# Performance work log

Measured on AMD Instinct MI355X. Metric: run time of the kernel, lower is better.

The kernel has to match this reference:

```python
import jax, jax.numpy as jnp
import numpy as np

IN_D = 512
VOCAB = 32000
SEQ = 2048

def setup_inputs() -> dict:
    key = jax.random.key(0)
    ks = jax.random.split(key, 12)
    d = IN_D
    def xavier(k, shape):
        fan_in, fan_out = shape[1], shape[0]
        a = jnp.sqrt(6.0 / (fan_in + fan_out))
        return jax.random.uniform(k, shape, jnp.float32, -a, a)
    return {
        'X': jax.random.randint(ks[0], (1, SEQ), 0, VOCAB),
        'wz': xavier(ks[1], (VOCAB, d)),
        'uz': xavier(ks[2], (d, d)),
        'w': xavier(ks[3], (VOCAB, d)),
        'u': xavier(ks[4], (d, d)),
        'wr': xavier(ks[5], (VOCAB, d)),
        'ur': xavier(ks[6], (d, d)),
        'wy': xavier(ks[7], (VOCAB, d)),
        'bz': xavier(ks[8], (1, d)),
        'br': xavier(ks[9], (1, d)),
        'bh': xavier(ks[10], (1, d)),
        'by': xavier(ks[11], (1, VOCAB)),
    }

def reference(X, wz, uz, w, u, wr, ur, wy, bz, br, bh, by):
    idx = X[0]                      # (T,) batch is hardcoded to 1 in original
    ez = wz[idx]                    # (T, d) per-step embedding gathers, done once
    er = wr[idx]
    eh = w[idx]

    def step(h, emb):
        e_z, e_r, e_h = emb
        z = jax.nn.sigmoid(e_z + h @ uz.T + bz[0])
        r = jax.nn.sigmoid(e_r + h @ ur.T + br[0])
        h_xh = jnp.tanh(e_h + (r * h) @ u.T + bh[0])
        h_new = h * z + (1.0 - z) * h_xh
        return h_new, h_new

    h0 = jnp.zeros((wz.shape[1],), dtype=wz.dtype)
    _, hs = jax.lax.scan(step, h0, (ez, er, eh))   # hs: (T, d)
    logits = hs @ wy.T + by[0]                     # (T, vocab)
    outs = jax.nn.log_softmax(logits, axis=-1)     # matches squeeze(0)
    hiddens = hs[None, :, :]                       # (1, T, d)
    return outs, hiddens
```

## Files before the change

### kernel.cpp

```cpp
#include <hip/hip_runtime.h>
#include <math.h>

typedef unsigned short u16;
typedef unsigned long long u64;
typedef unsigned short us8 __attribute__((ext_vector_type(8)));
typedef short bf16x8 __attribute__((ext_vector_type(8)));
typedef float f32x4 __attribute__((ext_vector_type(4)));

#define D       512
#define SEQ     2048
#define VOCAB   32000
#define NB      16
#define RPB     32
#define STPB    512

__device__ __forceinline__ u16 f2bf(float f) {
    union { float f; unsigned i; } x; x.f = f;
    unsigned r = x.i + 0x7fff + ((x.i >> 16) & 1);
    return (u16)(r >> 16);
}

__device__ __forceinline__ u64 tag_ld(const u64* p) {
    return __hip_atomic_load(p, __ATOMIC_RELAXED, __HIP_MEMORY_SCOPE_AGENT);
}
__device__ __forceinline__ void tag_st(u64* p, u64 v) {
    __hip_atomic_store(p, v, __ATOMIC_RELAXED, __HIP_MEMORY_SCOPE_AGENT);
}
__device__ __forceinline__ u64 packtv(float f, unsigned tag) {
    union { float f; unsigned i; } x; x.f = f;
    return ((u64)tag << 32) | (u64)x.i;
}
__device__ __forceinline__ float unpackv(u64 v) {
    union { unsigned i; float f; } x; x.i = (unsigned)v;
    return x.f;
}

__global__ void init_scratch(u64* __restrict__ hbuf, u64* __restrict__ rhbuf)
{
    const int t = threadIdx.x;
    hbuf[t]  = 0ull;
    rhbuf[t] = 0ull;
}

__global__ __launch_bounds__(STPB, 2) void scan_kernel(
    const int* __restrict__ X,
    const float* __restrict__ WZ, const float* __restrict__ UZ,
    const float* __restrict__ W,  const float* __restrict__ U,
    const float* __restrict__ WR, const float* __restrict__ UR,
    const float* __restrict__ BZ, const float* __restrict__ BR,
    const float* __restrict__ BH,
    u64* __restrict__ hbuf, u64* __restrict__ rhbuf,
    float* __restrict__ outH)
{
    __shared__ int   idxsm[SEQ];
    __shared__ float hsm[(D / 32) * 33];

    const int tid = threadIdx.x, b = blockIdx.x;
    const int r  = tid >> 4;
    const int cg = tid & 15;
    const int c0 = cg * 32;
    const int g  = b * RPB + r;

    for (int i = tid; i < SEQ; i += STPB) idxsm[i] = X[i];

    float uzw[32], urw[32], uw[32];
#pragma unroll
    for (int j = 0; j < 32; j += 4) {
        f32x4 vz = *(const f32x4*)&UZ[(size_t)g * D + c0 + j];
        f32x4 vr = *(const f32x4*)&UR[(size_t)g * D + c0 + j];
        f32x4 vu = *(const f32x4*)&U [(size_t)g * D + c0 + j];
#pragma unroll
        for (int q = 0; q < 4; ++q) {
            uzw[j + q] = vz[q];
            urw[j + q] = vr[q];
            uw [j + q] = vu[q];
        }
    }
    const float bzv = BZ[g], brv = BR[g], bhv = BH[g];
    __syncthreads();

    const int i0 = idxsm[0];
    float ezc = WZ[(size_t)i0 * D + g];
    float erc = WR[(size_t)i0 * D + g];
    float ehc = W [(size_t)i0 * D + g];

#pragma unroll 1
    for (int t = 0; t < SEQ; ++t) {
        const int tn = (t + 1 < SEQ) ? t + 1 : t;
        const int in_ = idxsm[tn];
        const float pz = WZ[(size_t)in_ * D + g];
        const float pr = WR[(size_t)in_ * D + g];
        const float ph = W [(size_t)in_ * D + g];
        const unsigned ta = (unsigned)t;
        const unsigned tb = (unsigned)t + 1u;

        if (tid < 128) {
            const int e = tid * 4;
            u64 v0, v1, v2, v3;
            for (;;) {
                v0 = tag_ld(&hbuf[e + 0]);
                v1 = tag_ld(&hbuf[e + 1]);
                v2 = tag_ld(&hbuf[e + 2]);
                v3 = tag_ld(&hbuf[e + 3]);
                if ((unsigned)(v0 >> 32) >= ta && (unsigned)(v1 >> 32) >= ta &&
                    (unsigned)(v2 >> 32) >= ta && (unsigned)(v3 >> 32) >= ta)
                    break;
            }
            float* p = &hsm[(e >> 5) * 33 + (e & 31)];
            p[0] = unpackv(v0); p[1] = unpackv(v1);
            p[2] = unpackv(v2); p[3] = unpackv(v3);
        }
        __syncthreads();

        float az = 0.f, ar = 0.f;
#pragma unroll
        for (int j = 0; j < 32; ++j) {
            float hj = hsm[cg * 33 + j];
            az = fmaf(uzw[j], hj, az);
            ar = fmaf(urw[j], hj, ar);
        }
#pragma unroll
        for (int mk = 8; mk; mk >>= 1) {
            az += __shfl_xor(az, mk);
            ar += __shfl_xor(ar, mk);
        }
        const float hrow = hsm[b * 33 + r];
        const float zz = 1.f / (1.f + __expf(-(ezc + az + bzv)));
        const float rr = 1.f / (1.f + __expf(-(erc + ar + brv)));
        if (cg == 0) tag_st(&rhbuf[g], packtv(rr * hrow, tb));
        __syncthreads();

        if (tid < 128) {
            const int e = tid * 4;
            u64 v0, v1, v2, v3;
            for (;;) {
                v0 = tag_ld(&rhbuf[e + 0]);
                v1 = tag_ld(&rhbuf[e + 1]);
                v2 = tag_ld(&rhbuf[e + 2]);
                v3 = tag_ld(&rhbuf[e + 3]);
                if ((unsigned)(v0 >> 32) >= tb && (unsigned)(v1 >> 32) >= tb &&
                    (unsigned)(v2 >> 32) >= tb && (unsigned)(v3 >> 32) >= tb)
                    break;
            }
            float* p = &hsm[(e >> 5) * 33 + (e & 31)];
            p[0] = unpackv(v0); p[1] = unpackv(v1);
            p[2] = unpackv(v2); p[3] = unpackv(v3);
        }
        __syncthreads();

        float ah = 0.f;
#pragma unroll
        for (int j = 0; j < 32; ++j) {
            float xj = hsm[cg * 33 + j];
            ah = fmaf(uw[j], xj, ah);
        }
#pragma unroll
        for (int mk = 8; mk; mk >>= 1) ah += __shfl_xor(ah, mk);

        const float hxh  = tanhf(ehc + ah + bhv);
        const float hnew = hrow * zz + (1.f - zz) * hxh;
        if (cg == 0) {
            tag_st(&hbuf[g], packtv(hnew, tb));
            outH[(size_t)t * D + g] = hnew;
        }
        __syncthreads();

        ezc = pz; erc = pr; ehc = ph;
    }
}

#define GBM 128
#define GBN 128
#define GBK 64

__global__ __launch_bounds__(256) void gemm_logits(
    const float* __restrict__ A,
    const float* __restrict__ B,
    const float* __restrict__ BY,
    float* __restrict__ C)
{
    __shared__ __align__(16) u16 As[GBM * GBK];
    __shared__ __align__(16) u16 Bs[GBN * GBK];

    const int tid = threadIdx.x;
    const int wv = tid >> 6, lane = tid & 63;
    const int lr = lane & 15, lg = lane >> 4;
    const int bm = blockIdx.y, bn = blockIdx.x;
    const int wm = (wv >> 1) * 64, wn = (wv & 1) * 64;

    const int srow = tid >> 3;
    const int scol = (tid & 7) * 8;

    f32x4 acc[4][4] = {};

    for (int kt = 0; kt < D; kt += GBK) {
        __syncthreads();
#pragma unroll
        for (int p = 0; p < 4; ++p) {
            const int row = p * 32 + srow;
            f32x4 a0 = *(const f32x4*)&A[(size_t)(bm * GBM + row) * D + kt + scol];
            f32x4 a1 = *(const f32x4*)&A[(size_t)(bm * GBM + row) * D + kt + scol + 4];
            f32x4 b0 = *(const f32x4*)&B[(size_t)(bn * GBN + row) * D + kt + scol];
            f32x4 b1 = *(const f32x4*)&B[(size_t)(bn * GBN + row) * D + kt + scol + 4];
            us8 oa, ob;
#pragma unroll
            for (int q = 0; q < 4; ++q) {
                oa[q] = f2bf(a0[q]); oa[4 + q] = f2bf(a1[q]);
                ob[q] = f2bf(b0[q]); ob[4 + q] = f2bf(b1[q]);
            }
            *(us8*)&As[row * GBK + scol] = oa;
            *(us8*)&Bs[row * GBK + scol] = ob;
        }
        __syncthreads();
#pragma unroll
        for (int kk = 0; kk < 2; ++kk) {
            bf16x8 af[4], bfr[4];
#pragma unroll
            for (int mi = 0; mi < 4; ++mi)
                af[mi] = *(const bf16x8*)&As[(wm + mi * 16 + lr) * GBK + kk * 32 + lg * 8];
#pragma unroll
            for (int ni = 0; ni < 4; ++ni)
                bfr[ni] = *(const bf16x8*)&Bs[(wn + ni * 16 + lr) * GBK + kk * 32 + lg * 8];
#pragma unroll
            for (int mi = 0; mi < 4; ++mi)
#pragma unroll
                for (int ni = 0; ni < 4; ++ni)
                    acc[mi][ni] = __builtin_amdgcn_mfma_f32_16x16x32_bf16(
                        af[mi], bfr[ni], acc[mi][ni], 0, 0, 0);
        }
    }

#pragma unroll
    for (int ni = 0; ni < 4; ++ni) {
        const int n = bn * GBN + wn + ni * 16 + lr;
        const float byv = BY[n];
#pragma unroll
        for (int mi = 0; mi < 4; ++mi) {
#pragma unroll
            for (int q = 0; q < 4; ++q) {
                const int m = bm * GBM + wm + mi * 16 + lg * 4 + q;
                C[(size_t)m * VOCAB + n] = acc[mi][ni][q] + byv;
            }
        }
    }
}

__global__ __launch_bounds__(256) void logsoftmax_kernel(float* __restrict__ C)
{
    const int m = blockIdx.x;
    float* row = C + (size_t)m * VOCAB;
    const int tid = threadIdx.x;

    float s = 0.f;
    for (int v = tid; v < VOCAB / 4; v += 256) {
        f32x4 x = *(const f32x4*)&row[v * 4];
        s += __expf(x[0]) + __expf(x[1]) + __expf(x[2]) + __expf(x[3]);
    }
#pragma unroll
    for (int mk = 32; mk; mk >>= 1) s += __shfl_xor(s, mk);
    __shared__ float red[4];
    if ((tid & 63) == 0) red[tid >> 6] = s;
    __syncthreads();
    const float lse = __logf(red[0] + red[1] + red[2] + red[3]);

    for (int v = tid; v < VOCAB / 4; v += 256) {
        f32x4 x = *(const f32x4*)&row[v * 4];
        x[0] -= lse; x[1] -= lse; x[2] -= lse; x[3] -= lse;
        *(f32x4*)&row[v * 4] = x;
    }
}

extern "C" void kernel_launch(void* const* d_in, const int* in_sizes, int n_in,
                              void* d_out, int out_size, void* d_ws, size_t ws_size,
                              hipStream_t stream)
{
    const int*   X  = (const int*)d_in[0];
    const float* wz = (const float*)d_in[1];
    const float* uz = (const float*)d_in[2];
    const float* w  = (const float*)d_in[3];
    const float* u  = (const float*)d_in[4];
    const float* wr = (const float*)d_in[5];
    const float* ur = (const float*)d_in[6];
    const float* wy = (const float*)d_in[7];
    const float* bz = (const float*)d_in[8];
    const float* br = (const float*)d_in[9];
    const float* bh = (const float*)d_in[10];
    const float* by = (const float*)d_in[11];

    float* out  = (float*)d_out;
    float* outH = out + (size_t)SEQ * VOCAB;

    char* scratch = (ws_size >= 8192) ? (char*)d_ws : (char*)d_out;
    u64* hbuf  = (u64*)scratch;
    u64* rhbuf = (u64*)(scratch + 4096);

    init_scratch<<<1, STPB, 0, stream>>>(hbuf, rhbuf);

    scan_kernel<<<NB, STPB, 0, stream>>>(X, wz, uz, w, u, wr, ur, bz, br, bh,
                                         hbuf, rhbuf, outH);

    dim3 ggrid(VOCAB / GBN, SEQ / GBM);
    gemm_logits<<<ggrid, 256, 0, stream>>>(outH, wy, by, out);

    logsoftmax_kernel<<<SEQ, 256, 0, stream>>>(out);
}
```

Before: 6.843 ms.

## Replace two cross-block handoffs per step with one partial-sum exchange

The scan step now has each block compute partial products of U with its own slice of r*h across all 512 outputs. It publishes those partials plus z*h and 1-z into a double-buffered tagged buffer. Every block then gathers all 16 partials and computes the full new h redundantly, so only one global exchange per timestep is needed instead of two. This also swaps __syncthreads for lighter LDS-only barriers and uses an exp-based tanh. In exchange, each thread polls 18 tagged words per step, which adds memory traffic and contention.

```diff
diff --git a/kernel.cpp b/kernel.cpp
--- a/kernel.cpp
+++ b/kernel.cpp
@@ -13,6 +13,8 @@
 #define NB      16
 #define RPB     32
 #define STPB    512
+#define PBSTR   576
+#define PBTOT   (2 * NB * PBSTR)
 
 __device__ __forceinline__ u16 f2bf(float f) {
     union { float f; unsigned i; } x; x.f = f;
@@ -34,12 +36,18 @@
     union { unsigned i; float f; } x; x.i = (unsigned)v;
     return x.f;
 }
-
-__global__ void init_scratch(u64* __restrict__ hbuf, u64* __restrict__ rhbuf)
-{
-    const int t = threadIdx.x;
-    hbuf[t]  = 0ull;
-    rhbuf[t] = 0ull;
+__device__ __forceinline__ float ftanh(float x) {
+    return 1.f - 2.f / (1.f + __expf(2.f * x));
+}
+__device__ __forceinline__ void bar_lds() {
+    asm volatile("s_waitcnt lgkmcnt(0)" ::: "memory");
+    __builtin_amdgcn_s_barrier();
+}
+
+__global__ void init_scratch(u64* __restrict__ pbuf)
+{
+    const int t = blockIdx.x * blockDim.x + threadIdx.x;
+    if (t < PBTOT) pbuf[t] = 0ull;
 }
 
 __global__ __launch_bounds__(STPB, 2) void scan_kernel(
@@ -49,68 +57,60 @@
     const float* __restrict__ WR, const float* __restrict__ UR,
     const float* __restrict__ BZ, const float* __restrict__ BR,
     const float* __restrict__ BH,
-    u64* __restrict__ hbuf, u64* __restrict__ rhbuf,
+    u64* __restrict__ pbuf,
     float* __restrict__ outH)
 {
     __shared__ int   idxsm[SEQ];
     __shared__ float hsm[(D / 32) * 33];
+    __shared__ float rhsm[RPB];
 
     const int tid = threadIdx.x, b = blockIdx.x;
     const int r  = tid >> 4;
     const int cg = tid & 15;
     const int c0 = cg * 32;
     const int g  = b * RPB + r;
-
-    for (int i = tid; i < SEQ; i += STPB) idxsm[i] = X[i];
-
-    float uzw[32], urw[32], uw[32];
+    const int i  = tid;
+
+    for (int k = tid; k < SEQ; k += STPB) idxsm[k] = X[k];
+
+    float uzw[32], urw[32], ucol[32];
 #pragma unroll
     for (int j = 0; j < 32; j += 4) {
         f32x4 vz = *(const f32x4*)&UZ[(size_t)g * D + c0 + j];
         f32x4 vr = *(const f32x4*)&UR[(size_t)g * D + c0 + j];
-        f32x4 vu = *(const f32x4*)&U [(size_t)g * D + c0 + j];
+        f32x4 vu = *(const f32x4*)&U [(size_t)i * D + b * RPB + j];
 #pragma unroll
         for (int q = 0; q < 4; ++q) {
-            uzw[j + q] = vz[q];
-            urw[j + q] = vr[q];
-            uw [j + q] = vu[q];
-        }
-    }
-    const float bzv = BZ[g], brv = BR[g], bhv = BH[g];
+            uzw[j + q]  = vz[q];
+            urw[j + q]  = vr[q];
+            ucol[j + q] = vu[q];
+        }
+    }
+    const float bzv = BZ[g], brv = BR[g], bhv = BH[i];
+
+    hsm[(i >> 5) * 33 + (i & 31)] = 0.f;
     __syncthreads();
 
     const int i0 = idxsm[0];
     float ezc = WZ[(size_t)i0 * D + g];
     float erc = WR[(size_t)i0 * D + g];
-    float ehc = W [(size_t)i0 * D + g];
+    float ehc = W [(size_t)i0 * D + i];
+
+    float hprev = 0.f;
+    u64* const pb0 = pbuf;
+    u64* const pb1 = pbuf + NB * PBSTR;
 
 #pragma unroll 1
     for (int t = 0; t < SEQ; ++t) {
+        if (t > 0 && (i >> 5) == b) outH[(size_t)(t - 1) * D + i] = hprev;
+
         const int tn = (t + 1 < SEQ) ? t + 1 : t;
         const int in_ = idxsm[tn];
         const float pz = WZ[(size_t)in_ * D + g];
         const float pr = WR[(size_t)in_ * D + g];
-        const float ph = W [(size_t)in_ * D + g];
-        const unsigned ta = (unsigned)t;
-        const unsigned tb = (unsigned)t + 1u;
-
-        if (tid < 128) {
-            const int e = tid * 4;
-            u64 v0, v1, v2, v3;
-            for (;;) {
-                v0 = tag_ld(&hbuf[e + 0]);
-                v1 = tag_ld(&hbuf[e + 1]);
-                v2 = tag_ld(&hbuf[e + 2]);
-                v3 = tag_ld(&hbuf[e + 3]);
-                if ((unsigned)(v0 >> 32) >= ta && (unsigned)(v1 >> 32) >= ta &&
-                    (unsigned)(v2 >> 32) >= ta && (unsigned)(v3 >> 32) >= ta)
-                    break;
-            }
-            float* p = &hsm[(e >> 5) * 33 + (e & 31)];
-            p[0] = unpackv(v0); p[1] = unpackv(v1);
-            p[2] = unpackv(v2); p[3] = unpackv(v3);
-        }
-        __syncthreads();
+        const float ph = W [(size_t)in_ * D + i];
+        const unsigned tt = (unsigned)t + 1u;
+        u64* const pb = (tt & 1u) ? pb1 : pb0;
 
         float az = 0.f, ar = 0.f;
 #pragma unroll
@@ -127,46 +127,45 @@
         const float hrow = hsm[b * 33 + r];
         const float zz = 1.f / (1.f + __expf(-(ezc + az + bzv)));
         const float rr = 1.f / (1.f + __expf(-(erc + ar + brv)));
-        if (cg == 0) tag_st(&rhbuf[g], packtv(rr * hrow, tb));
-        __syncthreads();
-
-        if (tid < 128) {
-            const int e = tid * 4;
-            u64 v0, v1, v2, v3;
-            for (;;) {
-                v0 = tag_ld(&rhbuf[e + 0]);
-                v1 = tag_ld(&rhbuf[e + 1]);
-                v2 = tag_ld(&rhbuf[e + 2]);
-                v3 = tag_ld(&rhbuf[e + 3]);
-                if ((unsigned)(v0 >> 32) >= tb && (unsigned)(v1 >> 32) >= tb &&
-                    (unsigned)(v2 >> 32) >= tb && (unsigned)(v3 >> 32) >= tb)
-                    break;
+        if (cg == 0) rhsm[r] = rr * hrow;
+        bar_lds();
+
+        float P = 0.f;
+#pragma unroll
+        for (int jl = 0; jl < 32; ++jl) P = fmaf(ucol[jl], rhsm[jl], P);
+        tag_st(&pb[b * PBSTR + i], packtv(P, tt));
+        if (cg == 0) {
+            tag_st(&pb[b * PBSTR + 512 + r], packtv(zz * hrow, tt));
+            tag_st(&pb[b * PBSTR + 544 + r], packtv(1.f - zz, tt));
+        }
+
+        u64 vP[NB], vzh, voz;
+        const int ow = i >> 5, il = i & 31;
+        for (;;) {
+            bool ok = true;
+#pragma unroll
+            for (int bb = 0; bb < NB; ++bb) {
+                vP[bb] = tag_ld(&pb[bb * PBSTR + i]);
+                ok &= ((unsigned)(vP[bb] >> 32) >= tt);
             }
-            float* p = &hsm[(e >> 5) * 33 + (e & 31)];
-            p[0] = unpackv(v0); p[1] = unpackv(v1);
-            p[2] = unpackv(v2); p[3] = unpackv(v3);
-        }
-        __syncthreads();
-
-        float ah = 0.f;
-#pragma unroll
-        for (int j = 0; j < 32; ++j) {
-            float xj = hsm[cg * 33 + j];
-            ah = fmaf(uw[j], xj, ah);
-        }
-#pragma unroll
-        for (int mk = 8; mk; mk >>= 1) ah += __shfl_xor(ah, mk);
-
-        const float hxh  = tanhf(ehc + ah + bhv);
-        const float hnew = hrow * zz + (1.f - zz) * hxh;
-        if (cg == 0) {
-            tag_st(&hbuf[g], packtv(hnew, tb));
-            outH[(size_t)t * D + g] = hnew;
-        }
-        __syncthreads();
+            vzh = tag_ld(&pb[ow * PBSTR + 512 + il]);
+            voz = tag_ld(&pb[ow * PBSTR + 544 + il]);
+            ok &= ((unsigned)(vzh >> 32) >= tt) & ((unsigned)(voz >> 32) >= tt);
+            if (ok) break;
+        }
+        float s = 0.f;
+#pragma unroll
+        for (int bb = 0; bb < NB; ++bb) s += unpackv(vP[bb]);
+        const float hxh  = ftanh(ehc + s + bhv);
+        const float hnew = unpackv(vzh) + unpackv(voz) * hxh;
+
+        hsm[(i >> 5) * 33 + (i & 31)] = hnew;
+        hprev = hnew;
+        bar_lds();
 
         ezc = pz; erc = pr; ehc = ph;
     }
+    if ((i >> 5) == b) outH[(size_t)(SEQ - 1) * D + i] = hprev;
 }
 
 #define GBM 128
@@ -290,14 +289,13 @@
     float* out  = (float*)d_out;
     float* outH = out + (size_t)SEQ * VOCAB;
 
-    char* scratch = (ws_size >= 8192) ? (char*)d_ws : (char*)d_out;
-    u64* hbuf  = (u64*)scratch;
-    u64* rhbuf = (u64*)(scratch + 4096);
-
-    init_scratch<<<1, STPB, 0, stream>>>(hbuf, rhbuf);
+    const size_t pbytes = (size_t)PBTOT * 8;
+    u64* pbuf = (ws_size >= pbytes) ? (u64*)d_ws : (u64*)d_out;
+
+    init_scratch<<<(PBTOT + STPB - 1) / STPB, STPB, 0, stream>>>(pbuf);
 
     scan_kernel<<<NB, STPB, 0, stream>>>(X, wz, uz, w, u, wr, ur, bz, br, bh,
-                                         hbuf, rhbuf, outH);
+                                         pbuf, outH);
 
     dim3 ggrid(VOCAB / GBN, SEQ / GBM);
     gemm_logits<<<ggrid, 256, 0, stream>>>(outH, wy, by, out);
```

After: 7.261 ms. 1.06x slower.
